# Optimization experiments

Measured on AMD Instinct MI355X. Metric: run time of the kernel, lower is better.

Reference implementation:

```python
import jax, jax.numpy as jnp
import numpy as np

J, L, A, A_PRIME, C_CH = 4, 4, 2, 2, 1
B, M, N = 4, 128, 128


def _compute_idx():
    # mirrors CorrLayerDownsample.compute_idx with delta_j=J, delta_l=L,
    # shift_mode='samec' and num_channels=1 (to_shift_color always True)
    dj, dl = J, L
    la1, la2, shifted = [], [], []
    for c1 in range(C_CH):
        for c2 in range(C_CH):
            for j1 in range(J):
                for j2 in range(j1, min(j1 + 1 + dj, J)):
                    for l1 in range(L):
                        for l2 in range(max(0, l1 + 1 - dl), min(L, l1 + 1 + dl)):
                            for a1 in range(A):
                                for a2 in range(A_PRIME):
                                    la1.append((j1, A * L * c1 + A * l1 + a1))
                                    la2.append((j2, A * L * c2 + A * l2 + a2))
                                    shifted.append(j2 + 1)
    return (np.asarray(la1, np.int32), np.asarray(la2, np.int32),
            np.asarray(shifted, np.int32))


def _make_masks():
    # stand-in for create_masks_shift: mask 0 = zero shift only; mask k (k>=1)
    # = wrapped square neighborhood of radius 2**(k-1) (shift scale grows with j2)
    xs = np.minimum(np.arange(M), M - np.arange(M))
    ys = np.minimum(np.arange(N), N - np.arange(N))
    masks = np.zeros((J + 1, M, N), np.float32)
    masks[0, 0, 0] = 1.0
    for k in range(1, J + 1):
        r = 2 ** (k - 1)
        masks[k] = ((xs[:, None] <= r) & (ys[None, :] <= r)).astype(np.float32)
    return masks


def setup_inputs() -> dict:
    key = jax.random.key(0)
    la1, la2, shifted = _compute_idx()
    masks = _make_masks()
    union_idx = np.where(masks.sum(0).reshape(-1) > 0)[0].astype(np.int32)
    xpsi = jax.random.normal(key, (J, B, C_CH * L * A, M, N), dtype=jnp.float32)
    return {
        "xpsi": xpsi,
        "masks_shift": jnp.asarray(masks),
        "la1": jnp.asarray(la1),
        "la2": jnp.asarray(la2),
        "shifted": jnp.asarray(shifted),
        "union_idx": jnp.asarray(union_idx),
    }


def reference(xpsi, masks_shift, la1, la2, shifted, union_idx):
    # xpsi: [J, B, C, M, N] real. FFT once per (scale, channel) map.
    hatx = jnp.fft.fft2(xpsi)                     # [J, B, C, M, N] complex64
    # gather the (scale, la-channel) pair for every moment (all scales same size,
    # so the per-(j1,j2) loop + upsample of the original collapses to one gather)
    h1 = hatx[la1[:, 0], :, la1[:, 1]]            # [P, B, M, N]
    h2 = hatx[la2[:, 0], :, la2[:, 1]]            # [P, B, M, N]
    corr = jnp.fft.ifft2(h1 * jnp.conj(h2)).real  # [P, B, M, N]
    masked = corr * masks_shift[shifted][:, None]  # per-moment shift mask
    P, Bb, Mm, Nn = masked.shape
    # flatten=True path: keep only positions in the union of all shift masks
    return masked.reshape(P, Bb, Mm * Nn)[:, :, union_idx]
```

## Files before the change

kernel.cpp:

```cpp
#include <hip/hip_runtime.h>

typedef __attribute__((ext_vector_type(8))) short short8;
typedef __attribute__((ext_vector_type(4))) float float4v;
typedef __attribute__((address_space(1))) const unsigned int gu32;
typedef __attribute__((address_space(3))) unsigned int lu32;

#define TPB 256
#define NXPSI (4*4*8*16384)
#define NGR   (NXPSI/4)
#define ZPG   64
#define PBYTE (NXPSI*2 + ZPG*8)
#define NPART 12828672
#define NOUT  739840
#define NTILE 34

__device__ __constant__ int TBASE[19] = {
    0, 1114112, 2228224, 3342336, 4456448, 5570560, 6684672, 7798784, 8912896,
    10027008, 10469376, 10911744, 11354112, 11796480,
    12238848, 12402688, 12566528,
    12730368, 12779520};

__device__ __constant__ unsigned char TN0[NTILE] = {
    0,0,16,16,32,32,48,48,64,64,80,80,96,96,112,112,128,128,
    0,0,16,16,32,32,48,48,64,64,
    0,16,32,
    0,8,16};
__device__ __constant__ unsigned char TMOFF[NTILE] = {
    0,16,0,16,0,16,0,16,0,16,0,16,0,16,0,16,0,16,
    0,16,0,16,0,16,0,16,0,16,
    0,0,0,
    0,0,0};
__device__ __constant__ unsigned char TGL[NTILE] = {
    0,0,1,1,2,2,3,3,4,4,5,5,6,6,7,7,8,8,
    9,9,10,10,11,11,12,12,13,13,
    14,15,16,
    17,17,18};

static __device__ __forceinline__ unsigned short f2bf(float f) {
    unsigned int u = __builtin_bit_cast(unsigned int, f);
    u = (u + 0x7FFFu + ((u >> 16) & 1u)) >> 16;
    return (unsigned short)u;
}

__global__ __launch_bounds__(256)
void conv_bf16(const float* __restrict__ in, unsigned short* __restrict__ outw) {
    const int g = blockIdx.x * 256 + threadIdx.x;
    if (g < NGR) {
        const float4 v = reinterpret_cast<const float4*>(in)[g];
        reinterpret_cast<ushort4*>(outw)[g] =
            ushort4{f2bf(v.x), f2bf(v.y), f2bf(v.z), f2bf(v.w)};
    } else if (g < NGR + ZPG) {
        reinterpret_cast<ushort4*>(outw)[g] = ushort4{0, 0, 0, 0};
    }
}

template<int J2, bool PRE, bool PART>
static __device__ __forceinline__ void corr_body(
        const float* __restrict__ xpsi, const unsigned short* __restrict__ xbf,
        float* __restrict__ out, float* __restrict__ part,
        unsigned char* smem, int tgl, int n0, int moff, int b, int kc)
{
    constexpr int R    = 1 << J2;
    constexpr int DXN  = 2 * R + 1;
    constexpr int DYN  = DXN;
    constexpr int MV   = 8 * (J2 + 1);
    constexpr int ROWS = 16 + 2 * R;
    constexpr int ABUF = 16 * 256;
    constexpr int S    = DYN * MV * 16;
    constexpr int W    = (J2 == 0) ? 8 : 16;

    unsigned short* a_lds = (unsigned short*)smem;
    unsigned short* b_lds = (unsigned short*)(smem + 4 * ABUF);

    const int k0    = kc * 16;
    const int vrows = (MV - moff < 16) ? MV - moff : 16;

    const int ch2lo = n0 / DXN;
    int nhi = n0 + W - 1; if (nhi > 8 * DXN - 1) nhi = 8 * DXN - 1;
    const int nimg = nhi / DXN - ch2lo + 1;

    const int tid  = threadIdx.x;
    const int lane = tid & 63;
    const int wv   = tid >> 6;
    const int c    = lane & 15;
    const int g    = lane >> 4;

    const int ncol    = n0 + c;
    const bool validn = (ncol < 8 * DXN) && (J2 > 0 || c < 8);
    const int ncc     = validn ? ncol : n0;
    const int ch2     = ncc / DXN;
    const int dxi     = ncc - ch2 * DXN;
    const int dx      = dxi - R;
    const int xo      = dx < 0 ? dx + 17 : dx;
    const int bst     = ((ch2 - ch2lo) * ROWS + (2 * R - dxi)) * 152;

    auto stageA = [&](int sub, int bufi) {
        unsigned short* ab = a_lds + bufi * ABUF;
        #pragma unroll
        for (int it = 0; it < 2; ++it) {
            const int o  = it * TPB + tid;
            const int ms = o >> 5;
            const int lo = (o & 31) ^ ms;
            const int me = moff + ms;
            const int j1 = me >> 3, ch1 = me & 7;
            if (PRE) {
                const unsigned short* src = (ms < vrows)
                    ? xbf + ((((size_t)j1*4 + b)*8) + ch1) * 16384
                          + (k0 + sub * 2 + (lo >> 4)) * 128 + ((lo & 15) << 3)
                    : xbf + NXPSI + ((lo & 31) << 3);
                __builtin_amdgcn_global_load_lds((gu32*)src, (lu32*)(ab + o * 8), 16, 0, 0);
            } else {
                ushort4 w0{0,0,0,0}, w1{0,0,0,0};
                if (ms < vrows) {
                    const float* s = xpsi + ((((size_t)j1*4 + b)*8) + ch1) * 16384
                                   + (k0 + sub * 2 + (lo >> 4)) * 128 + ((lo & 15) << 3);
                    const float4 f0 = ((const float4*)s)[0];
                    const float4 f1 = ((const float4*)s)[1];
                    w0 = ushort4{f2bf(f0.x), f2bf(f0.y), f2bf(f0.z), f2bf(f0.w)};
                    w1 = ushort4{f2bf(f1.x), f2bf(f1.y), f2bf(f1.z), f2bf(f1.w)};
                }
                *(ushort4*)(ab + o * 8)     = w0;
                *(ushort4*)(ab + o * 8 + 4) = w1;
            }
        }
    };

    stageA(0, 0);

    if (PRE && J2 >= 2) {
        for (int ci = 0; ci < nimg; ++ci) {
            const unsigned short* img = xbf + ((((size_t)J2*4 + b)*8) + ch2lo + ci) * 16384;
            const int ng2 = ROWS * 36;
            for (int i = tid; i < ng2; i += TPB) {
                const int tr = i / 36, tc = (i - tr * 36) * 4;
                const int sr = (k0 - R + tr) & 127;
                const int sc = (tc + R - 16) & 127;
                *(ushort4*)(b_lds + (ci * ROWS + tr) * 152 + tc) =
                    *(const ushort4*)(img + sr * 128 + sc);
            }
        }
    } else {
        const int tot = nimg * ROWS * 144;
        for (int i = tid; i < tot; i += TPB) {
            const int ci = i / (ROWS * 144);
            const int rr = i - ci * (ROWS * 144);
            const int tr = rr / 144, tc = rr - tr * 144;
            const int sr = (k0 - R + tr) & 127;
            const int sc = (tc + R - 16) & 127;
            b_lds[(ci * ROWS + tr) * 152 + tc] = PRE
                ? xbf[((((size_t)J2*4 + b)*8) + ch2lo + ci) * 16384 + sr * 128 + sc]
                : f2bf(xpsi[((((size_t)J2*4 + b)*8) + ch2lo + ci) * 16384 + sr * 128 + sc]);
        }
    }

    float4v acc[DYN];
    #pragma unroll
    for (int i = 0; i < DYN; ++i) acc[i] = (float4v)0.f;

    auto compute = [&](int sub, int bufi) {
        const char* abase = (const char*)(a_lds + bufi * ABUF);
        #pragma unroll
        for (int i2 = 0; i2 < 2; ++i2) {
            const int loff = (((i2 << 8) | (wv << 6) | (g << 4))) ^ (c << 4);
            const short8 af0 = *(const short8*)(abase + c * 512 + loff);

            const unsigned short* bp = b_lds + bst + (sub * 2 + i2) * 152
                                     + (wv << 5) + (g << 3);
            const uint4 wA = *(const uint4*)bp;
            const uint4 wB = *(const uint4*)(bp + 8);
            const uint4 wC = *(const uint4*)(bp + 16);
            const unsigned int wd[12] = {wA.x,wA.y,wA.z,wA.w, wB.x,wB.y,wB.z,wB.w,
                                         wC.x,wC.y,wC.z,wC.w};
            #pragma unroll
            for (int dyi = 0; dyi < DYN; ++dyi) {
                unsigned int o0, o1, o2, o3;
                if ((dyi & 1) == 0) {
                    const int bb = 8 - (dyi >> 1);
                    o0 = wd[bb]; o1 = wd[bb+1]; o2 = wd[bb+2]; o3 = wd[bb+3];
                } else {
                    const int bb = (15 - dyi) >> 1;
                    o0 = (wd[bb]   >> 16) | (wd[bb+1] << 16);
                    o1 = (wd[bb+1] >> 16) | (wd[bb+2] << 16);
                    o2 = (wd[bb+2] >> 16) | (wd[bb+3] << 16);
                    o3 = (wd[bb+3] >> 16) | (wd[bb+4] << 16);
                }
                union { unsigned int u[4]; short8 s; } bq;
                bq.u[0] = o0; bq.u[1] = o1; bq.u[2] = o2; bq.u[3] = o3;
                acc[dyi] = __builtin_amdgcn_mfma_f32_16x16x32_bf16(
                    af0, bq.s, acc[dyi], 0, 0, 0);
            }
        }
    };

    __syncthreads();
    for (int sub = 0; sub < 8; ++sub) {
        if (sub < 7) stageA(sub + 1, (sub + 1) & 1);
        compute(sub, sub & 1);
        __syncthreads();
    }

    if (!validn) return;
    const int cpart = (n0 & 15) + c;

    if (PART) {
        float* pt = part + TBASE[tgl] + (size_t)((kc * 4 + wv) * 4 + b) * S;
        #pragma unroll
        for (int dyi = 0; dyi < DYN; ++dyi) {
            #pragma unroll
            for (int t2 = 0; t2 < 4; ++t2) {
                const int ml = (g << 2) + t2;
                if (ml >= vrows) continue;
                pt[(dyi * MV + moff + ml) * 16 + cpart] = acc[dyi][t2];
            }
        }
    } else {
        #pragma unroll
        for (int dyi = 0; dyi < DYN; ++dyi) {
            const int dy = dyi - R;
            const int yo = dy < 0 ? dy + 17 : dy;
            #pragma unroll
            for (int t2 = 0; t2 < 4; ++t2) {
                const int ml = (g << 2) + t2;
                if (ml >= vrows) continue;
                const int m = moff + ml;
                const int j1 = m >> 3, ch1 = m & 7;
                const int pb = ((j1 * (9 - j1)) >> 1) + (J2 - j1);
                const int p  = pb * 64 + ((ch1 >> 1) << 4) + ((ch2 >> 1) << 2)
                             + ((ch1 & 1) << 1) + (ch2 & 1);
                atomicAdd(out + (size_t)(p * 4 + b) * 289 + xo * 17 + yo, acc[dyi][t2]);
            }
        }
    }
}

template<bool PRE, bool PART>
__global__ __launch_bounds__(TPB, 3)
void corr_v6(const float* __restrict__ xpsi, const unsigned short* __restrict__ xbf,
             float* __restrict__ out, float* __restrict__ part)
{
    __shared__ __align__(16) unsigned char smem[40704];
    const int bid = blockIdx.x;
    const int t   = bid % NTILE;
    const int rem = bid / NTILE;
    const int b   = rem & 3;
    const int kc  = rem >> 2;
    const int n0   = TN0[t];
    const int moff = TMOFF[t];
    const int tgl  = TGL[t];
    if (t < 18)      corr_body<3, PRE, PART>(xpsi, xbf, out, part, smem, tgl, n0, moff, b, kc);
    else if (t < 28) corr_body<2, PRE, PART>(xpsi, xbf, out, part, smem, tgl, n0, moff, b, kc);
    else if (t < 31) corr_body<1, PRE, PART>(xpsi, xbf, out, part, smem, tgl, n0, moff, b, kc);
    else             corr_body<0, PRE, PART>(xpsi, xbf, out, part, smem, tgl, n0, moff, b, kc);
}

__global__ __launch_bounds__(256)
void reduce2(const float* __restrict__ part, float* __restrict__ out)
{
    const int t  = blockIdx.y;
    const int j2 = (t < 9) ? 3 : (t < 14) ? 2 : (t < 17) ? 1 : 0;
    const int nt = t - ((t < 9) ? 0 : (t < 14) ? 9 : (t < 17) ? 14 : 17);
    const int R = 1 << j2, DXN = 2 * R + 1, DYN = DXN, MV = 8 * (j2 + 1);
    const int S = DYN * MV * 16;
    const int tot = 4 * DYN * MV * 4;
    const int i = blockIdx.x * 256 + threadIdx.x;
    if (i >= tot) return;
    const int c4 = (i & 3) << 2;
    int r2 = i >> 2;
    const int m = r2 % MV;  r2 /= MV;
    const int dyi = r2 % DYN;
    const int b   = r2 / DYN;
    const int ncol0 = nt * 16 + c4;
    if (ncol0 >= 8 * DXN) return;
    const float* q = part + TBASE[t] + (size_t)b * S + (dyi * MV + m) * 16 + c4;
    float4 v = {0.f, 0.f, 0.f, 0.f};
    for (int qq = 0; qq < 32; ++qq) {
        const float4 w = *(const float4*)(q + (size_t)qq * 4 * S);
        v.x += w.x; v.y += w.y; v.z += w.z; v.w += w.w;
    }
    const int dy = dyi - R;
    const int yo = dy < 0 ? dy + 17 : dy;
    const int j1 = m >> 3, ch1 = m & 7;
    const int pb = ((j1 * (9 - j1)) >> 1) + (j2 - j1);
    const float vv[4] = {v.x, v.y, v.z, v.w};
    #pragma unroll
    for (int e = 0; e < 4; ++e) {
        const int ncol = ncol0 + e;
        if (ncol >= 8 * DXN) break;
        const int ch2 = ncol / DXN;
        const int dxi = ncol - ch2 * DXN;
        const int dx  = dxi - R;
        const int xo  = dx < 0 ? dx + 17 : dx;
        const int p   = pb * 64 + ((ch1 >> 1) << 4) + ((ch2 >> 1) << 2)
                      + ((ch1 & 1) << 1) + (ch2 & 1);
        out[(size_t)(p * 4 + b) * 289 + xo * 17 + yo] = vv[e];
    }
}

extern "C" void kernel_launch(void* const* d_in, const int* in_sizes, int n_in,
                              void* d_out, int out_size, void* d_ws, size_t ws_size,
                              hipStream_t stream) {
    const float* xpsi = (const float*)d_in[0];
    float* out = (float*)d_out;

    if (ws_size >= (size_t)PBYTE + (size_t)NPART * 4) {
        unsigned short* xbf = (unsigned short*)d_ws;
        float* part = (float*)((char*)d_ws + PBYTE);
        hipMemsetAsync(d_out, 0, (size_t)out_size * sizeof(float), stream);
        conv_bf16<<<(NGR + ZPG + 255) / 256, 256, 0, stream>>>(xpsi, xbf);
        corr_v6<true, true><<<NTILE * 32, TPB, 0, stream>>>(xpsi, xbf, out, part);
        reduce2<<<dim3(34, 19), 256, 0, stream>>>(part, out);
    } else if (ws_size >= (size_t)PBYTE) {
        unsigned short* xbf = (unsigned short*)d_ws;
        hipMemsetAsync(d_out, 0, (size_t)out_size * sizeof(float), stream);
        conv_bf16<<<(NGR + ZPG + 255) / 256, 256, 0, stream>>>(xpsi, xbf);
        corr_v6<true, false><<<NTILE * 32, TPB, 0, stream>>>(xpsi, xbf, out, nullptr);
    } else {
        hipMemsetAsync(d_out, 0, (size_t)out_size * sizeof(float), stream);
        corr_v6<false, false><<<NTILE * 32, TPB, 0, stream>>>(xpsi, nullptr, out, nullptr);
    }
}
```

Before: 52.48 us.

## Reduce the four waves' partial sums in shared memory before writing partials

```diff
diff --git a/kernel.cpp b/kernel.cpp
--- a/kernel.cpp
+++ b/kernel.cpp
@@ -10,15 +10,15 @@
 #define NGR   (NXPSI/4)
 #define ZPG   64
 #define PBYTE (NXPSI*2 + ZPG*8)
-#define NPART 12828672
+#define NPART 3207168
 #define NOUT  739840
 #define NTILE 34
 
 __device__ __constant__ int TBASE[19] = {
-    0, 1114112, 2228224, 3342336, 4456448, 5570560, 6684672, 7798784, 8912896,
-    10027008, 10469376, 10911744, 11354112, 11796480,
-    12238848, 12402688, 12566528,
-    12730368, 12779520};
+    0, 278528, 557056, 835584, 1114112, 1392640, 1671168, 1949696, 2228224,
+    2506752, 2617344, 2727936, 2838528, 2949120,
+    3059712, 3100672, 3141632,
+    3182592, 3194880};
 
 __device__ __constant__ unsigned char TN0[NTILE] = {
     0,0,16,16,32,32,48,48,64,64,80,80,96,96,112,112,128,128,
@@ -199,43 +199,68 @@
         __syncthreads();
     }
 
+    if (PART) {
+        constexpr int NG  = (DYN < 9) ? DYN : 9;
+        constexpr int NPH = (DYN + NG - 1) / NG;
+        float* red = (float*)smem;
+        float* pt  = part + TBASE[tgl] + (size_t)(kc * 4 + b) * S;
+        const int cpart0 = n0 & 15;
+        #pragma unroll
+        for (int ph = 0; ph < NPH; ++ph) {
+            const int d0 = ph * NG;
+            const int nd = (DYN - d0 < NG) ? (DYN - d0) : NG;
+            __syncthreads();
+            #pragma unroll
+            for (int dl = 0; dl < NG; ++dl) {
+                if (dl >= nd) break;
+                *(float4v*)(red + ((wv * NG + dl) * 64 + lane) * 4) = acc[d0 + dl];
+            }
+            __syncthreads();
+            for (int i = tid; i < nd * 64; i += TPB) {
+                const int dl = i >> 6;
+                const int ln = i & 63;
+                const float4v s0 = *(const float4v*)(red + ((0 * NG + dl) * 64 + ln) * 4);
+                const float4v s1 = *(const float4v*)(red + ((1 * NG + dl) * 64 + ln) * 4);
+                const float4v s2 = *(const float4v*)(red + ((2 * NG + dl) * 64 + ln) * 4);
+                const float4v s3 = *(const float4v*)(red + ((3 * NG + dl) * 64 + ln) * 4);
+                const float4v s = (s0 + s1) + (s2 + s3);
+                const int cc = ln & 15, gg = ln >> 4;
+                if ((n0 + cc < 8 * DXN) && (J2 > 0 || cc < 8)) {
+                    const int dyi = d0 + dl;
+                    #pragma unroll
+                    for (int t2 = 0; t2 < 4; ++t2) {
+                        const int ml = (gg << 2) + t2;
+                        if (ml < vrows)
+                            pt[(dyi * MV + moff + ml) * 16 + cpart0 + cc] = s[t2];
+                    }
+                }
+            }
+        }
+        return;
+    }
+
     if (!validn) return;
-    const int cpart = (n0 & 15) + c;
-
-    if (PART) {
-        float* pt = part + TBASE[tgl] + (size_t)((kc * 4 + wv) * 4 + b) * S;
+    #pragma unroll
+    for (int dyi = 0; dyi < DYN; ++dyi) {
+        const int dy = dyi - R;
+        const int yo = dy < 0 ? dy + 17 : dy;
         #pragma unroll
-        for (int dyi = 0; dyi < DYN; ++dyi) {
-            #pragma unroll
-            for (int t2 = 0; t2 < 4; ++t2) {
-                const int ml = (g << 2) + t2;
-                if (ml >= vrows) continue;
-                pt[(dyi * MV + moff + ml) * 16 + cpart] = acc[dyi][t2];
-            }
-        }
-    } else {
-        #pragma unroll
-        for (int dyi = 0; dyi < DYN; ++dyi) {
-            const int dy = dyi - R;
-            const int yo = dy < 0 ? dy + 17 : dy;
-            #pragma unroll
-            for (int t2 = 0; t2 < 4; ++t2) {
-                const int ml = (g << 2) + t2;
-                if (ml >= vrows) continue;
-                const int m = moff + ml;
-                const int j1 = m >> 3, ch1 = m & 7;
-                const int pb = ((j1 * (9 - j1)) >> 1) + (J2 - j1);
-                const int p  = pb * 64 + ((ch1 >> 1) << 4) + ((ch2 >> 1) << 2)
-                             + ((ch1 & 1) << 1) + (ch2 & 1);
-                atomicAdd(out + (size_t)(p * 4 + b) * 289 + xo * 17 + yo, acc[dyi][t2]);
-            }
+        for (int t2 = 0; t2 < 4; ++t2) {
+            const int ml = (g << 2) + t2;
+            if (ml >= vrows) continue;
+            const int m = moff + ml;
+            const int j1 = m >> 3, ch1 = m & 7;
+            const int pb = ((j1 * (9 - j1)) >> 1) + (J2 - j1);
+            const int p  = pb * 64 + ((ch1 >> 1) << 4) + ((ch2 >> 1) << 2)
+                         + ((ch1 & 1) << 1) + (ch2 & 1);
+            atomicAdd(out + (size_t)(p * 4 + b) * 289 + xo * 17 + yo, acc[dyi][t2]);
         }
     }
 }
 
 template<bool PRE, bool PART>
 __global__ __launch_bounds__(TPB, 3)
-void corr_v6(const float* __restrict__ xpsi, const unsigned short* __restrict__ xbf,
+void corr_v7(const float* __restrict__ xpsi, const unsigned short* __restrict__ xbf,
              float* __restrict__ out, float* __restrict__ part)
 {
     __shared__ __align__(16) unsigned char smem[40704];
@@ -273,7 +298,8 @@
     if (ncol0 >= 8 * DXN) return;
     const float* q = part + TBASE[t] + (size_t)b * S + (dyi * MV + m) * 16 + c4;
     float4 v = {0.f, 0.f, 0.f, 0.f};
-    for (int qq = 0; qq < 32; ++qq) {
+    #pragma unroll
+    for (int qq = 0; qq < 8; ++qq) {
         const float4 w = *(const float4*)(q + (size_t)qq * 4 * S);
         v.x += w.x; v.y += w.y; v.z += w.z; v.w += w.w;
     }
@@ -307,15 +333,15 @@
         float* part = (float*)((char*)d_ws + PBYTE);
         hipMemsetAsync(d_out, 0, (size_t)out_size * sizeof(float), stream);
         conv_bf16<<<(NGR + ZPG + 255) / 256, 256, 0, stream>>>(xpsi, xbf);
-        corr_v6<true, true><<<NTILE * 32, TPB, 0, stream>>>(xpsi, xbf, out, part);
+        corr_v7<true, true><<<NTILE * 32, TPB, 0, stream>>>(xpsi, xbf, out, part);
         reduce2<<<dim3(34, 19), 256, 0, stream>>>(part, out);
     } else if (ws_size >= (size_t)PBYTE) {
         unsigned short* xbf = (unsigned short*)d_ws;
         hipMemsetAsync(d_out, 0, (size_t)out_size * sizeof(float), stream);
         conv_bf16<<<(NGR + ZPG + 255) / 256, 256, 0, stream>>>(xpsi, xbf);
-        corr_v6<true, false><<<NTILE * 32, TPB, 0, stream>>>(xpsi, xbf, out, nullptr);
+        corr_v7<true, false><<<NTILE * 32, TPB, 0, stream>>>(xpsi, xbf, out, nullptr);
     } else {
         hipMemsetAsync(d_out, 0, (size_t)out_size * sizeof(float), stream);
-        corr_v6<false, false><<<NTILE * 32, TPB, 0, stream>>>(xpsi, nullptr, out, nullptr);
-    }
-}
+        corr_v7<false, false><<<NTILE * 32, TPB, 0, stream>>>(xpsi, nullptr, out, nullptr);
+    }
+}
```

Result: faster. 47.03 us (-10.4%).
